# Performance work log

Measured on AMD Instinct MI355X. Metric: run time of the kernel, lower is better.

The kernel has to match this reference:

```python
import jax, jax.numpy as jnp
import numpy as np

B, C, HZ, SX = 512, 112, 8, 16
P = HZ * HZ   # num_kernel = 64 template pixels
OC = 256
EPS = 1e-5

def _conv(x, w, pad, groups=1):
    return jax.lax.conv_general_dilated(
        x, w, (1, 1), [(pad, pad), (pad, pad)],
        feature_group_count=groups,
        dimension_numbers=('NCHW', 'OIHW', 'NCHW'))

def _bn(x, g, b, m, v):
    # eval-mode BatchNorm2d with running stats
    scale = (g / jnp.sqrt(v + EPS))[None, :, None, None]
    return (x - m[None, :, None, None]) * scale + b[None, :, None, None]

def setup_inputs() -> dict:
    key = jax.random.key(0)
    ks = jax.random.split(key, 16)
    n = lambda i, shape, s=0.05: jax.random.normal(ks[i], shape, dtype=jnp.float32) * s
    return dict(
        search=jax.random.normal(ks[0], (B, C, SX, SX), dtype=jnp.float32),
        kernel=jax.random.normal(ks[1], (B, C, HZ, HZ), dtype=jnp.float32),
        ca_w1=n(2, (P, P)), ca_b1=jnp.zeros((P,), jnp.float32),
        ca_w2=n(3, (P, P)), ca_b2=jnp.zeros((P,), jnp.float32),
        cls_dw=n(4, (P, 1, 3, 3)), cls_pw=n(5, (OC, P)),
        cls_bn_g=jnp.ones((OC,), jnp.float32), cls_bn_b=jnp.zeros((OC,), jnp.float32),
        cls_bn_m=n(6, (OC,)), cls_bn_v=jax.random.uniform(ks[7], (OC,), jnp.float32, 0.5, 1.5),
        cls_pred_w=n(8, (1, OC, 3, 3)), cls_pred_b=jnp.zeros((1,), jnp.float32),
        box_dw=n(9, (P, 1, 3, 3)), box_pw=n(10, (OC, P)),
        box_bn_g=jnp.ones((OC,), jnp.float32), box_bn_b=jnp.zeros((OC,), jnp.float32),
        box_bn_m=n(11, (OC,)), box_bn_v=jax.random.uniform(ks[12], (OC,), jnp.float32, 0.5, 1.5),
        box_pred_w=n(13, (4, OC, 3, 3)), box_pred_b=jnp.zeros((4,), jnp.float32),
        adjust=0.1 * jnp.ones((1,), jnp.float32),
        bias_p=jnp.ones((1, 4, 1, 1), jnp.float32),
    )

def reference(search, kernel, ca_w1, ca_b1, ca_w2, ca_b2,
              cls_dw, cls_pw, cls_bn_g, cls_bn_b, cls_bn_m, cls_bn_v,
              cls_pred_w, cls_pred_b,
              box_dw, box_pw, box_bn_g, box_bn_b, box_bn_m, box_bn_v,
              box_pred_w, box_pred_b, adjust, bias_p):
    b, c, h, w = search.shape
    # pixel-wise correlation (batched form of the per-sample F.conv2d loop):
    # corr[b,p,i,j] = sum_c kernel[b,c].flatten()[p] * search[b,c,i,j]
    z = kernel.reshape(b, c, -1)                       # [B, C, P]
    corr = jnp.einsum('bcp,bcij->bpij', z, search)      # [B, P, H, W]
    # channel attention (CAModule, reduction=1)
    s = corr.mean(axis=(2, 3))                          # [B, P]
    a = jax.nn.sigmoid(jax.nn.relu(s @ ca_w1.T + ca_b1) @ ca_w2.T + ca_b2)
    corr = corr * a[:, :, None, None]
    # cls tower: depthwise 3x3 -> pointwise -> BN -> ReLU
    cfeat = jnp.einsum('oc,bchw->bohw', cls_pw, _conv(corr, cls_dw, 1, groups=P))
    cfeat = jax.nn.relu(_bn(cfeat, cls_bn_g, cls_bn_b, cls_bn_m, cls_bn_v))
    cls = 0.1 * (_conv(cfeat, cls_pred_w, 1) + cls_pred_b[None, :, None, None])
    # bbox tower
    rfeat = jnp.einsum('oc,bchw->bohw', box_pw, _conv(corr, box_dw, 1, groups=P))
    rfeat = jax.nn.relu(_bn(rfeat, box_bn_g, box_bn_b, box_bn_m, box_bn_v))
    pred = _conv(rfeat, box_pred_w, 1) + box_pred_b[None, :, None, None]
    x = jnp.exp(adjust[0] * pred + bias_p)
    return (x, cls)
```

## Files before the change

### kernel.cpp

```cpp
#include <hip/hip_runtime.h>
#include <hip/hip_bf16.h>


typedef __attribute__((ext_vector_type(8))) short  bf16x8;
typedef __attribute__((ext_vector_type(4))) float  f32x4;

union U8 { bf16x8 v; uint4 q; unsigned short u[8]; };

__device__ __forceinline__ float bf2f(unsigned short h){
  union { unsigned int u; float f; } c; c.u = ((unsigned int)h) << 16; return c.f;
}
__device__ __forceinline__ unsigned short f2bf(float f){
  union { float f; unsigned int u; } c; c.f = f;
  unsigned int r = (c.u + 0x7FFFu + ((c.u >> 16) & 1u)) >> 16;
  return (unsigned short)r;
}
__device__ __forceinline__ unsigned int f2bf2(float lo, float hi){
  return (unsigned int)f2bf(lo) | ((unsigned int)f2bf(hi) << 16);
}

__device__ __forceinline__ int swz(int row, int pix){
  return row*256 + (((pix>>3) ^ (row&31))<<3) + (pix&7);
}
__device__ __forceinline__ int zt_off(int p, int c){
  return (p<<8) + ((((c>>3) ^ (p&15)) & 15)<<4) + ((c&7)<<1);
}
__device__ __forceinline__ int sT_off(int pix, int c){
  return (pix<<7) + ((((c>>3) ^ (pix&7) ^ ((pix>>3)&7)) & 7)<<4) + ((c&7)<<1);
}
__device__ __forceinline__ int dT_off(int pix, int p){
  return (pix<<7) + (((((p>>3) ^ pix) & 7)) << 4) + ((p & 7) << 1);
}
__device__ __forceinline__ int fT_off(int pix, int ocl){
  return (pix<<6) + ((((ocl>>3) ^ pix ^ (pix>>2)) & 3) << 4) + ((ocl & 7) << 1);
}
__device__ __forceinline__ int pA_off(int ocl, int p){
  return (ocl<<7) + (((((p>>3) ^ ocl) & 7)) << 4) + ((p & 7) << 1);
}

__device__ __forceinline__ void stage_pw(int tid, int oc0,
                                         const float* __restrict__ pw,
                                         unsigned char* __restrict__ dst){
  const int ocl = tid >> 4, p0 = (tid & 15) << 2;
  const float4 f0 = *(const float4*)&pw[(oc0 + ocl)*64 + p0];
  uint2 w; w.x = f2bf2(f0.x, f0.y); w.y = f2bf2(f0.z, f0.w);
  *(uint2*)(dst + pA_off(ocl, p0)) = w;
}

template<int NOUT>
__device__ __forceinline__ void stage_wA(int tid, int oc0,
                                         const float* __restrict__ pdw,
                                         unsigned char* __restrict__ dst){
  #pragma unroll
  for (int i=0;i<(NOUT*288+511)/512;++i){
    const int idx = i*512 + tid;
    if (idx < NOUT*288){
      const int o   = idx / 288;
      const int rem = idx - o*288;
      const int tau = rem >> 5, ocl = rem & 31;
      *(unsigned short*)(dst + (idx<<1)) =
          f2bf(pdw[(o*256 + oc0 + ocl)*9 + tau]);
    }
  }
}

template<int NOUT>
__device__ __forceinline__ void run_tower(
    int tid, float ap,
    const float* __restrict__ dw,  const float* __restrict__ pw,
    const float* __restrict__ bng, const float* __restrict__ bnb,
    const float* __restrict__ bnm, const float* __restrict__ bnv,
    const float* __restrict__ pdw, const float* __restrict__ pdb,
    float* __restrict__ outp, float adj, const float* __restrict__ biasp,
    unsigned char* smem)
{
  const int lane = tid & 63, wave = tid >> 6;
  const int l15 = lane & 15, lg = lane >> 4;
  unsigned short* sA16 = (unsigned short*)smem;

  {
    const int p = lane;
    unsigned char* dT = smem + 32768;
    float wd[9];
    #pragma unroll
    for (int k=0;k<9;++k) wd[k] = dw[p*9+k] * ap;
    #pragma unroll
    for (int io=0;io<2;++io){
      const int ir = wave*2 + io;
      float ot[16];
      #pragma unroll
      for (int j=0;j<16;++j) ot[j] = 0.f;
      #pragma unroll
      for (int dr=0;dr<3;++dr){
        const int r = ir-1+dr;
        if (r >= 0 && r < 16){
          unsigned short tr[16];
          *(uint4*)&tr[0] = *(uint4*)&sA16[swz(p, r*16)];
          *(uint4*)&tr[8] = *(uint4*)&sA16[swz(p, r*16 + 8)];
          float rr[16];
          #pragma unroll
          for (int j=0;j<16;++j) rr[j] = bf2f(tr[j]);
          const float w0 = wd[dr*3+0], w1 = wd[dr*3+1], w2 = wd[dr*3+2];
          #pragma unroll
          for (int j=0;j<16;++j){
            float s = w1*rr[j];
            if (j > 0)  s = fmaf(w0, rr[j-1], s);
            if (j < 15) s = fmaf(w2, rr[j+1], s);
            ot[j] += s;
          }
        }
      }
      #pragma unroll
      for (int j=0;j<16;++j)
        *(unsigned short*)(dT + dT_off(ir*16+j, p)) = f2bf(ot[j]);
    }
  }
  __syncthreads();

  U8 bfr[2][2];
  #pragma unroll
  for (int nt=0;nt<2;++nt)
    #pragma unroll
    for (int ks=0;ks<2;++ks)
      bfr[nt][ks].q = *(const uint4*)(smem + 32768 +
          dT_off(wave*32 + nt*16 + l15, ks*32 + lg*8));
  __syncthreads();

  float* scl = (float*)(smem + 61952);
  float* bia = (float*)(smem + 62976);
  if (tid < 256){
    const float s = bng[tid] * rsqrtf(bnv[tid] + 1e-5f);
    scl[tid] = s;
    bia[tid] = bnb[tid] - bnm[tid]*s;
  }
  stage_pw(tid, 0, pw, smem + 49152);
  stage_wA<NOUT>(tid, 0, pdw, smem + 57344);

  f32x4 accp[2];
  #pragma unroll
  for (int nt=0;nt<2;++nt) accp[nt] = f32x4{0.f,0.f,0.f,0.f};

  for (int ch=0; ch<8; ++ch){
    const int buf = ch & 1, oc0 = ch*32;
    __syncthreads();

    unsigned char* pAb = smem + 49152 + buf*4096;
    U8 af[2][2];
    #pragma unroll
    for (int mt=0;mt<2;++mt)
      #pragma unroll
      for (int ks=0;ks<2;++ks)
        af[mt][ks].q = *(const uint4*)(pAb + pA_off(mt*16 + l15, ks*32 + lg*8));
    f32x4 accw[2][2];
    #pragma unroll
    for (int mt=0;mt<2;++mt)
      #pragma unroll
      for (int nt=0;nt<2;++nt) accw[mt][nt] = f32x4{0.f,0.f,0.f,0.f};
    #pragma unroll
    for (int nt=0;nt<2;++nt){
      #pragma unroll
      for (int mt=0;mt<2;++mt){
        accw[mt][nt] = __builtin_amdgcn_mfma_f32_16x16x32_bf16(
            af[mt][0].v, bfr[nt][0].v, accw[mt][nt], 0, 0, 0);
        accw[mt][nt] = __builtin_amdgcn_mfma_f32_16x16x32_bf16(
            af[mt][1].v, bfr[nt][1].v, accw[mt][nt], 0, 0, 0);
      }
    }
    #pragma unroll
    for (int mt=0;mt<2;++mt){
      #pragma unroll
      for (int r=0;r<4;++r){
        const int ocl = mt*16 + lg*4 + r;
        const float sc = scl[oc0+ocl], bi = bia[oc0+ocl];
        #pragma unroll
        for (int nt=0;nt<2;++nt){
          const int pix = wave*32 + nt*16 + l15;
          const float v = fmaxf(fmaf(accw[mt][nt][r], sc, bi), 0.f);
          *(unsigned short*)(smem + 32768 + fT_off(pix, ocl)) = f2bf(v);
        }
      }
    }
    __syncthreads();

    unsigned char* wAb = smem + 57344 + buf*2304;
    #pragma unroll
    for (int dr=0;dr<3;++dr){
      #pragma unroll
      for (int dc=0;dc<3;++dc){
        const int tau = dr*3 + dc;
        U8 a;
        const int mr = (NOUT == 4) ? (l15 & 3) : 0;
        a.q = *(const uint4*)(wAb + ((mr*288 + tau*32 + lg*8) << 1));
        if (l15 >= NOUT) a.q = make_uint4(0u,0u,0u,0u);
        #pragma unroll
        for (int nt=0;nt<2;++nt){
          const int rp = wave*2 + nt + dr - 1;
          if (rp >= 0 && rp <= 15){
            const int cp = l15 + dc - 1;
            const int cc = cp < 0 ? 0 : (cp > 15 ? 15 : cp);
            U8 bf;
            bf.q = *(const uint4*)(smem + 32768 + fT_off(rp*16 + cc, lg*8));
            if (cp != cc) bf.q = make_uint4(0u,0u,0u,0u);
            accp[nt] = __builtin_amdgcn_mfma_f32_16x16x32_bf16(
                a.v, bf.v, accp[nt], 0, 0, 0);
          }
        }
      }
    }
    if (ch < 7){
      stage_pw(tid, oc0 + 32, pw, smem + 49152 + (buf^1)*4096);
      stage_wA<NOUT>(tid, oc0 + 32, pdw, smem + 57344 + (buf^1)*2304);
    }
  }

  if (lane < 16){
    #pragma unroll
    for (int nt=0;nt<2;++nt){
      const int rt = wave*2 + nt;
      if constexpr (NOUT == 1){
        outp[rt*16 + lane] = 0.1f*(accp[nt][0] + pdb[0]);
      } else {
        #pragma unroll
        for (int o=0;o<4;++o)
          outp[o*256 + rt*16 + lane] =
              expf(fmaf(adj, accp[nt][o] + pdb[o], biasp[o]));
      }
    }
  }
  __syncthreads();
}

__global__ __launch_bounds__(512, 4) void fused_head(
  const float* __restrict__ search, const float* __restrict__ kern,
  const float* __restrict__ ca_w1, const float* __restrict__ ca_b1,
  const float* __restrict__ ca_w2, const float* __restrict__ ca_b2,
  const float* __restrict__ cls_dw, const float* __restrict__ cls_pw,
  const float* __restrict__ cls_bn_g, const float* __restrict__ cls_bn_b,
  const float* __restrict__ cls_bn_m, const float* __restrict__ cls_bn_v,
  const float* __restrict__ cls_pred_w, const float* __restrict__ cls_pred_b,
  const float* __restrict__ box_dw, const float* __restrict__ box_pw,
  const float* __restrict__ box_bn_g, const float* __restrict__ box_bn_b,
  const float* __restrict__ box_bn_m, const float* __restrict__ box_bn_v,
  const float* __restrict__ box_pred_w, const float* __restrict__ box_pred_b,
  const float* __restrict__ adjust, const float* __restrict__ bias_p,
  float* __restrict__ out)
{
  __shared__ __align__(16) unsigned char smem[65536];
  const int b   = blockIdx.x;
  const int tid = threadIdx.x;
  const int lane = tid & 63, wave = tid >> 6;
  const int l15 = lane & 15, lg = lane >> 4;

  unsigned char* zb = smem;
  {
    const float* kb = kern + (size_t)b*7168;
    #pragma unroll
    for (int i=0;i<14;++i){
      const int idx = i*512 + tid;
      const int c = idx>>6, p = idx&63;
      *(unsigned short*)(zb + zt_off(p,c)) = f2bf(kb[idx]);
    }
    #pragma unroll
    for (int i=0;i<2;++i){
      const int idx = i*512 + tid;
      const int p = idx>>4, c = 112 + (idx&15);
      *(unsigned short*)(zb + zt_off(p,c)) = 0;
    }
  }

  unsigned char* stb = smem + 16384;
  const float* sea = search + (size_t)b*28672;
  f32x4 acc[4][2];
  #pragma unroll
  for (int mt=0;mt<4;++mt)
    #pragma unroll
    for (int nt=0;nt<2;++nt) acc[mt][nt] = f32x4{0.f,0.f,0.f,0.f};

  for (int kc=0;kc<2;++kc){
    __syncthreads();
    #pragma unroll
    for (int i=0;i<8;++i){
      const int f4i = i*512 + tid;
      const int cc = f4i>>6, pix0 = (f4i&63)<<2;
      const int c  = kc*64 + cc;
      float4 v;
      if (c < 112) v = *(const float4*)(sea + c*256 + pix0);
      else         v = make_float4(0.f,0.f,0.f,0.f);
      const float vv[4] = {v.x, v.y, v.z, v.w};
      #pragma unroll
      for (int j=0;j<4;++j)
        *(unsigned short*)(stb + sT_off(pix0+j, cc)) = f2bf(vv[j]);
    }
    __syncthreads();
    #pragma unroll
    for (int kt=0;kt<2;++kt){
      U8 bh[2];
      #pragma unroll
      for (int nt=0;nt<2;++nt){
        const int pix = wave*32 + nt*16 + l15;
        bh[nt].q = *(const uint4*)(stb + sT_off(pix, kt*32 + lg*8));
      }
      #pragma unroll
      for (int mt=0;mt<4;++mt){
        U8 ah;
        ah.q = *(const uint4*)(zb + zt_off(mt*16 + l15, kc*64 + kt*32 + lg*8));
        #pragma unroll
        for (int nt=0;nt<2;++nt)
          acc[mt][nt] = __builtin_amdgcn_mfma_f32_16x16x32_bf16(
              ah.v, bh[nt].v, acc[mt][nt], 0, 0, 0);
      }
    }
  }
  __syncthreads();

  unsigned short* sA16 = (unsigned short*)smem;
  #pragma unroll
  for (int mt=0;mt<4;++mt){
    #pragma unroll
    for (int nt=0;nt<2;++nt){
      const int pix = wave*32 + nt*16 + l15;
      #pragma unroll
      for (int r=0;r<4;++r)
        sA16[swz(mt*16 + lg*4 + r, pix)] = f2bf(acc[mt][nt][r]);
    }
  }

  float* ws    = (float*)(smem + 49152);
  float* smean = (float*)(smem + 51200);
  float* h1    = (float*)(smem + 51456);
  float* attvG = (float*)(smem + 51712);
  #pragma unroll
  for (int mt=0;mt<4;++mt){
    #pragma unroll
    for (int r=0;r<4;++r){
      float s = acc[mt][0][r] + acc[mt][1][r];
      s += __shfl_xor(s, 1, 64);
      s += __shfl_xor(s, 2, 64);
      s += __shfl_xor(s, 4, 64);
      s += __shfl_xor(s, 8, 64);
      if (l15 == 0) ws[wave*64 + mt*16 + lg*4 + r] = s;
    }
  }
  __syncthreads();
  if (tid < 64){
    float m = 0.f;
    #pragma unroll
    for (int w=0;w<8;++w) m += ws[w*64 + tid];
    smean[tid] = m * (1.f/256.f);
  }
  __syncthreads();
  if (tid < 64){
    float s = ca_b1[tid];
    const float* wr = ca_w1 + tid*64;
    #pragma unroll 8
    for (int k=0;k<64;++k) s += smean[k]*wr[k];
    h1[tid] = fmaxf(s, 0.f);
  }
  __syncthreads();
  if (tid < 64){
    float s = ca_b2[tid];
    const float* wr = ca_w2 + tid*64;
    #pragma unroll 8
    for (int k=0;k<64;++k) s += h1[k]*wr[k];
    attvG[tid] = 1.f/(1.f + expf(-s));
  }
  __syncthreads();
  const float ap = attvG[lane];

  const float adj = adjust[0];

  run_tower<1>(tid, ap, cls_dw, cls_pw, cls_bn_g, cls_bn_b, cls_bn_m,
               cls_bn_v, cls_pred_w, cls_pred_b,
               out + 524288 + (size_t)b*256, adj, bias_p, smem);
  run_tower<4>(tid, ap, box_dw, box_pw, box_bn_g, box_bn_b, box_bn_m,
               box_bn_v, box_pred_w, box_pred_b,
               out + (size_t)b*1024, adj, bias_p, smem);
}

extern "C" void kernel_launch(void* const* d_in, const int* in_sizes, int n_in,
                              void* d_out, int out_size, void* d_ws, size_t ws_size,
                              hipStream_t stream) {
  (void)in_sizes; (void)n_in; (void)d_ws; (void)ws_size; (void)out_size;
  const float* search     = (const float*)d_in[0];
  const float* kern       = (const float*)d_in[1];
  const float* ca_w1      = (const float*)d_in[2];
  const float* ca_b1      = (const float*)d_in[3];
  const float* ca_w2      = (const float*)d_in[4];
  const float* ca_b2      = (const float*)d_in[5];
  const float* cls_dw     = (const float*)d_in[6];
  const float* cls_pw     = (const float*)d_in[7];
  const float* cls_bn_g   = (const float*)d_in[8];
  const float* cls_bn_b   = (const float*)d_in[9];
  const float* cls_bn_m   = (const float*)d_in[10];
  const float* cls_bn_v   = (const float*)d_in[11];
  const float* cls_pred_w = (const float*)d_in[12];
  const float* cls_pred_b = (const float*)d_in[13];
  const float* box_dw     = (const float*)d_in[14];
  const float* box_pw     = (const float*)d_in[15];
  const float* box_bn_g   = (const float*)d_in[16];
  const float* box_bn_b   = (const float*)d_in[17];
  const float* box_bn_m   = (const float*)d_in[18];
  const float* box_bn_v   = (const float*)d_in[19];
  const float* box_pred_w = (const float*)d_in[20];
  const float* box_pred_b = (const float*)d_in[21];
  const float* adjust     = (const float*)d_in[22];
  const float* bias_p     = (const float*)d_in[23];

  hipLaunchKernelGGL(fused_head, dim3(512), dim3(512), 0, stream,
    search, kern, ca_w1, ca_b1, ca_w2, ca_b2,
    cls_dw, cls_pw, cls_bn_g, cls_bn_b, cls_bn_m, cls_bn_v,
    cls_pred_w, cls_pred_b,
    box_dw, box_pw, box_bn_g, box_bn_b, box_bn_m, box_bn_v,
    box_pred_w, box_pred_b, adjust, bias_p,
    (float*)d_out);
}
```

Before: 71.70 us.

## Run cls and box towers concurrently on separate halves of the block

Both depthwise convolutions still use all 512 threads, one after the other. The pointwise, BN and pred-conv stages of the two towers now run at the same time, with threads 0-255 handling cls and 256-511 handling box. Each half uses its own shared-memory regions for features, weights and BN parameters, and each wave covers 64 pixels instead of 32. The aim is to cut the number of serial chunk loops and barriers by overlapping the two towers. In exchange, the block is load-imbalanced because the box half does about four times the pred work, and register pressure per thread rises.

```diff
diff --git a/kernel.cpp b/kernel.cpp
--- a/kernel.cpp
+++ b/kernel.cpp
@@ -38,196 +38,68 @@
   return (ocl<<7) + (((((p>>3) ^ ocl) & 7)) << 4) + ((p & 7) << 1);
 }
 
-__device__ __forceinline__ void stage_pw(int tid, int oc0,
-                                         const float* __restrict__ pw,
-                                         unsigned char* __restrict__ dst){
-  const int ocl = tid >> 4, p0 = (tid & 15) << 2;
+__device__ __forceinline__ void depthwise(
+    int lane, int wave, float ap, const float* __restrict__ dw,
+    const unsigned short* __restrict__ sA16, unsigned char* __restrict__ dst)
+{
+  const int p = lane;
+  float wd[9];
+  #pragma unroll
+  for (int k=0;k<9;++k) wd[k] = dw[p*9+k] * ap;
+  #pragma unroll
+  for (int io=0;io<2;++io){
+    const int ir = wave*2 + io;
+    float ot[16];
+    #pragma unroll
+    for (int j=0;j<16;++j) ot[j] = 0.f;
+    #pragma unroll
+    for (int dr=0;dr<3;++dr){
+      const int r = ir-1+dr;
+      if (r >= 0 && r < 16){
+        unsigned short tr[16];
+        *(uint4*)&tr[0] = *(uint4*)&sA16[swz(p, r*16)];
+        *(uint4*)&tr[8] = *(uint4*)&sA16[swz(p, r*16 + 8)];
+        float rr[16];
+        #pragma unroll
+        for (int j=0;j<16;++j) rr[j] = bf2f(tr[j]);
+        const float w0 = wd[dr*3+0], w1 = wd[dr*3+1], w2 = wd[dr*3+2];
+        #pragma unroll
+        for (int j=0;j<16;++j){
+          float s = w1*rr[j];
+          if (j > 0)  s = fmaf(w0, rr[j-1], s);
+          if (j < 15) s = fmaf(w2, rr[j+1], s);
+          ot[j] += s;
+        }
+      }
+    }
+    #pragma unroll
+    for (int j=0;j<16;++j)
+      *(unsigned short*)(dst + dT_off(ir*16+j, p)) = f2bf(ot[j]);
+  }
+}
+
+__device__ __forceinline__ void stage_pw256(int t, int oc0,
+                                            const float* __restrict__ pw,
+                                            unsigned char* __restrict__ dst){
+  const int ocl = t >> 3, p0 = (t & 7) << 3;
   const float4 f0 = *(const float4*)&pw[(oc0 + ocl)*64 + p0];
-  uint2 w; w.x = f2bf2(f0.x, f0.y); w.y = f2bf2(f0.z, f0.w);
-  *(uint2*)(dst + pA_off(ocl, p0)) = w;
-}
-
-template<int NOUT>
-__device__ __forceinline__ void stage_wA(int tid, int oc0,
-                                         const float* __restrict__ pdw,
-                                         unsigned char* __restrict__ dst){
-  #pragma unroll
-  for (int i=0;i<(NOUT*288+511)/512;++i){
-    const int idx = i*512 + tid;
-    if (idx < NOUT*288){
-      const int o   = idx / 288;
-      const int rem = idx - o*288;
-      const int tau = rem >> 5, ocl = rem & 31;
-      *(unsigned short*)(dst + (idx<<1)) =
-          f2bf(pdw[(o*256 + oc0 + ocl)*9 + tau]);
-    }
-  }
-}
-
-template<int NOUT>
-__device__ __forceinline__ void run_tower(
-    int tid, float ap,
-    const float* __restrict__ dw,  const float* __restrict__ pw,
-    const float* __restrict__ bng, const float* __restrict__ bnb,
-    const float* __restrict__ bnm, const float* __restrict__ bnv,
-    const float* __restrict__ pdw, const float* __restrict__ pdb,
-    float* __restrict__ outp, float adj, const float* __restrict__ biasp,
-    unsigned char* smem)
-{
-  const int lane = tid & 63, wave = tid >> 6;
-  const int l15 = lane & 15, lg = lane >> 4;
-  unsigned short* sA16 = (unsigned short*)smem;
-
-  {
-    const int p = lane;
-    unsigned char* dT = smem + 32768;
-    float wd[9];
-    #pragma unroll
-    for (int k=0;k<9;++k) wd[k] = dw[p*9+k] * ap;
-    #pragma unroll
-    for (int io=0;io<2;++io){
-      const int ir = wave*2 + io;
-      float ot[16];
-      #pragma unroll
-      for (int j=0;j<16;++j) ot[j] = 0.f;
-      #pragma unroll
-      for (int dr=0;dr<3;++dr){
-        const int r = ir-1+dr;
-        if (r >= 0 && r < 16){
-          unsigned short tr[16];
-          *(uint4*)&tr[0] = *(uint4*)&sA16[swz(p, r*16)];
-          *(uint4*)&tr[8] = *(uint4*)&sA16[swz(p, r*16 + 8)];
-          float rr[16];
-          #pragma unroll
-          for (int j=0;j<16;++j) rr[j] = bf2f(tr[j]);
-          const float w0 = wd[dr*3+0], w1 = wd[dr*3+1], w2 = wd[dr*3+2];
-          #pragma unroll
-          for (int j=0;j<16;++j){
-            float s = w1*rr[j];
-            if (j > 0)  s = fmaf(w0, rr[j-1], s);
-            if (j < 15) s = fmaf(w2, rr[j+1], s);
-            ot[j] += s;
-          }
-        }
-      }
-      #pragma unroll
-      for (int j=0;j<16;++j)
-        *(unsigned short*)(dT + dT_off(ir*16+j, p)) = f2bf(ot[j]);
-    }
-  }
-  __syncthreads();
-
-  U8 bfr[2][2];
-  #pragma unroll
-  for (int nt=0;nt<2;++nt)
-    #pragma unroll
-    for (int ks=0;ks<2;++ks)
-      bfr[nt][ks].q = *(const uint4*)(smem + 32768 +
-          dT_off(wave*32 + nt*16 + l15, ks*32 + lg*8));
-  __syncthreads();
-
-  float* scl = (float*)(smem + 61952);
-  float* bia = (float*)(smem + 62976);
-  if (tid < 256){
-    const float s = bng[tid] * rsqrtf(bnv[tid] + 1e-5f);
-    scl[tid] = s;
-    bia[tid] = bnb[tid] - bnm[tid]*s;
-  }
-  stage_pw(tid, 0, pw, smem + 49152);
-  stage_wA<NOUT>(tid, 0, pdw, smem + 57344);
-
-  f32x4 accp[2];
-  #pragma unroll
-  for (int nt=0;nt<2;++nt) accp[nt] = f32x4{0.f,0.f,0.f,0.f};
-
-  for (int ch=0; ch<8; ++ch){
-    const int buf = ch & 1, oc0 = ch*32;
-    __syncthreads();
-
-    unsigned char* pAb = smem + 49152 + buf*4096;
-    U8 af[2][2];
-    #pragma unroll
-    for (int mt=0;mt<2;++mt)
-      #pragma unroll
-      for (int ks=0;ks<2;++ks)
-        af[mt][ks].q = *(const uint4*)(pAb + pA_off(mt*16 + l15, ks*32 + lg*8));
-    f32x4 accw[2][2];
-    #pragma unroll
-    for (int mt=0;mt<2;++mt)
-      #pragma unroll
-      for (int nt=0;nt<2;++nt) accw[mt][nt] = f32x4{0.f,0.f,0.f,0.f};
-    #pragma unroll
-    for (int nt=0;nt<2;++nt){
-      #pragma unroll
-      for (int mt=0;mt<2;++mt){
-        accw[mt][nt] = __builtin_amdgcn_mfma_f32_16x16x32_bf16(
-            af[mt][0].v, bfr[nt][0].v, accw[mt][nt], 0, 0, 0);
-        accw[mt][nt] = __builtin_amdgcn_mfma_f32_16x16x32_bf16(
-            af[mt][1].v, bfr[nt][1].v, accw[mt][nt], 0, 0, 0);
-      }
-    }
-    #pragma unroll
-    for (int mt=0;mt<2;++mt){
-      #pragma unroll
-      for (int r=0;r<4;++r){
-        const int ocl = mt*16 + lg*4 + r;
-        const float sc = scl[oc0+ocl], bi = bia[oc0+ocl];
-        #pragma unroll
-        for (int nt=0;nt<2;++nt){
-          const int pix = wave*32 + nt*16 + l15;
-          const float v = fmaxf(fmaf(accw[mt][nt][r], sc, bi), 0.f);
-          *(unsigned short*)(smem + 32768 + fT_off(pix, ocl)) = f2bf(v);
-        }
-      }
-    }
-    __syncthreads();
-
-    unsigned char* wAb = smem + 57344 + buf*2304;
-    #pragma unroll
-    for (int dr=0;dr<3;++dr){
-      #pragma unroll
-      for (int dc=0;dc<3;++dc){
-        const int tau = dr*3 + dc;
-        U8 a;
-        const int mr = (NOUT == 4) ? (l15 & 3) : 0;
-        a.q = *(const uint4*)(wAb + ((mr*288 + tau*32 + lg*8) << 1));
-        if (l15 >= NOUT) a.q = make_uint4(0u,0u,0u,0u);
-        #pragma unroll
-        for (int nt=0;nt<2;++nt){
-          const int rp = wave*2 + nt + dr - 1;
-          if (rp >= 0 && rp <= 15){
-            const int cp = l15 + dc - 1;
-            const int cc = cp < 0 ? 0 : (cp > 15 ? 15 : cp);
-            U8 bf;
-            bf.q = *(const uint4*)(smem + 32768 + fT_off(rp*16 + cc, lg*8));
-            if (cp != cc) bf.q = make_uint4(0u,0u,0u,0u);
-            accp[nt] = __builtin_amdgcn_mfma_f32_16x16x32_bf16(
-                a.v, bf.v, accp[nt], 0, 0, 0);
-          }
-        }
-      }
-    }
-    if (ch < 7){
-      stage_pw(tid, oc0 + 32, pw, smem + 49152 + (buf^1)*4096);
-      stage_wA<NOUT>(tid, oc0 + 32, pdw, smem + 57344 + (buf^1)*2304);
-    }
-  }
-
-  if (lane < 16){
-    #pragma unroll
-    for (int nt=0;nt<2;++nt){
-      const int rt = wave*2 + nt;
-      if constexpr (NOUT == 1){
-        outp[rt*16 + lane] = 0.1f*(accp[nt][0] + pdb[0]);
-      } else {
-        #pragma unroll
-        for (int o=0;o<4;++o)
-          outp[o*256 + rt*16 + lane] =
-              expf(fmaf(adj, accp[nt][o] + pdb[o], biasp[o]));
-      }
-    }
-  }
-  __syncthreads();
+  const float4 f1 = *(const float4*)&pw[(oc0 + ocl)*64 + p0 + 4];
+  U8 w;
+  w.u[0]=f2bf(f0.x); w.u[1]=f2bf(f0.y); w.u[2]=f2bf(f0.z); w.u[3]=f2bf(f0.w);
+  w.u[4]=f2bf(f1.x); w.u[5]=f2bf(f1.y); w.u[6]=f2bf(f1.z); w.u[7]=f2bf(f1.w);
+  *(uint4*)(dst + pA_off(ocl, p0)) = w.q;
+}
+
+__device__ __forceinline__ void stage_wA256(int t, int oc0, int nout,
+                                            const float* __restrict__ pdw,
+                                            unsigned char* __restrict__ dst){
+  for (int idx = t; idx < nout*288; idx += 256){
+    const int o   = idx / 288;
+    const int rem = idx - o*288;
+    const int tau = rem >> 5, ocl = rem & 31;
+    *(unsigned short*)(dst + (idx<<1)) =
+        f2bf(pdw[(o*256 + oc0 + ocl)*9 + tau]);
+  }
 }
 
 __global__ __launch_bounds__(512, 4) void fused_head(
@@ -366,15 +238,157 @@
   }
   __syncthreads();
   const float ap = attvG[lane];
+  __syncthreads();
 
   const float adj = adjust[0];
 
-  run_tower<1>(tid, ap, cls_dw, cls_pw, cls_bn_g, cls_bn_b, cls_bn_m,
-               cls_bn_v, cls_pred_w, cls_pred_b,
-               out + 524288 + (size_t)b*256, adj, bias_p, smem);
-  run_tower<4>(tid, ap, box_dw, box_pw, box_bn_g, box_bn_b, box_bn_m,
-               box_bn_v, box_pred_w, box_pred_b,
-               out + (size_t)b*1024, adj, bias_p, smem);
+  const int half = tid >> 8;
+  const int ttid = tid & 255;
+  const int wt   = wave & 3;
+  const int nout = half ? 4 : 1;
+
+  const float* pwp  = half ? box_pw     : cls_pw;
+  const float* bngp = half ? box_bn_g   : cls_bn_g;
+  const float* bnbp = half ? box_bn_b   : cls_bn_b;
+  const float* bnmp = half ? box_bn_m   : cls_bn_m;
+  const float* bnvp = half ? box_bn_v   : cls_bn_v;
+  const float* pdwp = half ? box_pred_w : cls_pred_w;
+  const float* pdbp = half ? box_pred_b : cls_pred_b;
+  float* outp = half ? (out + (size_t)b*1024)
+                     : (out + 524288 + (size_t)b*256);
+
+  unsigned char* dT = smem + 32768;
+
+  depthwise(lane, wave, ap, cls_dw, sA16, dT);
+  __syncthreads();
+  U8 bfr[4][2];
+  if (half == 0){
+    #pragma unroll
+    for (int nt=0;nt<4;++nt)
+      #pragma unroll
+      for (int ks=0;ks<2;++ks)
+        bfr[nt][ks].q = *(const uint4*)(dT +
+            dT_off(wt*64 + nt*16 + l15, ks*32 + lg*8));
+  }
+  __syncthreads();
+  depthwise(lane, wave, ap, box_dw, sA16, dT);
+  __syncthreads();
+  if (half == 1){
+    #pragma unroll
+    for (int nt=0;nt<4;++nt)
+      #pragma unroll
+      for (int ks=0;ks<2;++ks)
+        bfr[nt][ks].q = *(const uint4*)(dT +
+            dT_off(wt*64 + nt*16 + l15, ks*32 + lg*8));
+  }
+  __syncthreads();
+
+  unsigned char* featb = smem + half*16384;
+  unsigned char* pwb0  = smem + 32768 + half*8192;
+  unsigned char* wab0  = smem + (half ? 50304 : 49152);
+  const int wstride = nout*576;
+  float* scl = (float*)(smem + 55296 + half*2048);
+  float* bia = scl + 256;
+
+  {
+    const float s = bngp[ttid] * rsqrtf(bnvp[ttid] + 1e-5f);
+    scl[ttid] = s;
+    bia[ttid] = bnbp[ttid] - bnmp[ttid]*s;
+  }
+  stage_pw256(ttid, 0, pwp, pwb0);
+  stage_wA256(ttid, 0, nout, pdwp, wab0);
+
+  f32x4 accp[4];
+  #pragma unroll
+  for (int nt=0;nt<4;++nt) accp[nt] = f32x4{0.f,0.f,0.f,0.f};
+
+  for (int ch=0; ch<8; ++ch){
+    const int buf = ch & 1, oc0 = ch*32;
+    __syncthreads();
+
+    unsigned char* pAb = pwb0 + buf*4096;
+    U8 af[2][2];
+    #pragma unroll
+    for (int mt=0;mt<2;++mt)
+      #pragma unroll
+      for (int ks=0;ks<2;++ks)
+        af[mt][ks].q = *(const uint4*)(pAb + pA_off(mt*16 + l15, ks*32 + lg*8));
+    f32x4 accw[2][4];
+    #pragma unroll
+    for (int mt=0;mt<2;++mt)
+      #pragma unroll
+      for (int nt=0;nt<4;++nt) accw[mt][nt] = f32x4{0.f,0.f,0.f,0.f};
+    #pragma unroll
+    for (int nt=0;nt<4;++nt){
+      #pragma unroll
+      for (int mt=0;mt<2;++mt){
+        accw[mt][nt] = __builtin_amdgcn_mfma_f32_16x16x32_bf16(
+            af[mt][0].v, bfr[nt][0].v, accw[mt][nt], 0, 0, 0);
+        accw[mt][nt] = __builtin_amdgcn_mfma_f32_16x16x32_bf16(
+            af[mt][1].v, bfr[nt][1].v, accw[mt][nt], 0, 0, 0);
+      }
+    }
+    #pragma unroll
+    for (int mt=0;mt<2;++mt){
+      #pragma unroll
+      for (int r=0;r<4;++r){
+        const int ocl = mt*16 + lg*4 + r;
+        const float sc = scl[oc0+ocl], bi = bia[oc0+ocl];
+        #pragma unroll
+        for (int nt=0;nt<4;++nt){
+          const int pix = wt*64 + nt*16 + l15;
+          const float v = fmaxf(fmaf(accw[mt][nt][r], sc, bi), 0.f);
+          *(unsigned short*)(featb + fT_off(pix, ocl)) = f2bf(v);
+        }
+      }
+    }
+    __syncthreads();
+
+    unsigned char* wAb = wab0 + buf*wstride;
+    #pragma unroll
+    for (int dr=0;dr<3;++dr){
+      #pragma unroll
+      for (int dc=0;dc<3;++dc){
+        const int tau = dr*3 + dc;
+        U8 a;
+        const int mr = (nout == 4) ? (l15 & 3) : 0;
+        a.q = *(const uint4*)(wAb + ((mr*288 + tau*32 + lg*8) << 1));
+        if (l15 >= nout) a.q = make_uint4(0u,0u,0u,0u);
+        #pragma unroll
+        for (int nt=0;nt<4;++nt){
+          const int rp = wt*4 + nt + dr - 1;
+          if (rp >= 0 && rp <= 15){
+            const int cp = l15 + dc - 1;
+            const int cc = cp < 0 ? 0 : (cp > 15 ? 15 : cp);
+            U8 bf;
+            bf.q = *(const uint4*)(featb + fT_off(rp*16 + cc, lg*8));
+            if (cp != cc) bf.q = make_uint4(0u,0u,0u,0u);
+            accp[nt] = __builtin_amdgcn_mfma_f32_16x16x32_bf16(
+                a.v, bf.v, accp[nt], 0, 0, 0);
+          }
+        }
+      }
+    }
+    if (ch < 7){
+      stage_pw256(ttid, oc0 + 32, pwp, pwb0 + (buf^1)*4096);
+      stage_wA256(ttid, oc0 + 32, nout, pdwp, wab0 + (buf^1)*wstride);
+    }
+  }
+
+  if (lane < 16){
+    #pragma unroll
+    for (int nt=0;nt<4;++nt){
+      const int rt = wt*4 + nt;
+      if (nout == 1){
+        outp[rt*16 + lane] = 0.1f*(accp[nt][0] + pdbp[0]);
+      } else {
+        #pragma unroll
+        for (int o=0;o<4;++o)
+          outp[o*256 + rt*16 + lane] =
+              expf(fmaf(adj, accp[nt][o] + pdbp[o], bias_p[o]));
+      }
+    }
+  }
 }
 
 extern "C" void kernel_launch(void* const* d_in, const int* in_sizes, int n_in,
```

After: 77.18 us. 1.08x slower.

## Software-pipeline pointwise and 3x3 pred stages with double-buffered feature tiles

Applied to the files above, without the earlier changes.

The pointwise+BN+ReLU chunk for the next 32 output channels is now computed into a second feature buffer while the 3x3 prediction MFMAs consume the current one. This removes one barrier per chunk. The correlation tile is kept in registers as packed bf16 and rewritten to shared memory at the start of each tower, which frees shared space for the second feature buffer. In exchange it raises register pressure and adds an LDS rewrite per tower.

```diff
diff --git a/kernel.cpp b/kernel.cpp
--- a/kernel.cpp
+++ b/kernel.cpp
@@ -66,7 +66,7 @@
 
 template<int NOUT>
 __device__ __forceinline__ void run_tower(
-    int tid, float ap,
+    int tid, float ap, const unsigned int pk[16],
     const float* __restrict__ dw,  const float* __restrict__ pw,
     const float* __restrict__ bng, const float* __restrict__ bnb,
     const float* __restrict__ bnm, const float* __restrict__ bnv,
@@ -77,6 +77,22 @@
   const int lane = tid & 63, wave = tid >> 6;
   const int l15 = lane & 15, lg = lane >> 4;
   unsigned short* sA16 = (unsigned short*)smem;
+
+  #pragma unroll
+  for (int mt=0;mt<4;++mt){
+    #pragma unroll
+    for (int nt=0;nt<2;++nt){
+      const int pix = wave*32 + nt*16 + l15;
+      #pragma unroll
+      for (int rp=0;rp<2;++rp){
+        const unsigned int v = pk[(mt*2+nt)*2+rp];
+        const int p = mt*16 + lg*4 + rp*2;
+        sA16[swz(p,   pix)] = (unsigned short)(v & 0xffffu);
+        sA16[swz(p+1, pix)] = (unsigned short)(v >> 16);
+      }
+    }
+  }
+  __syncthreads();
 
   {
     const int p = lane;
@@ -133,41 +149,30 @@
     scl[tid] = s;
     bia[tid] = bnb[tid] - bnm[tid]*s;
   }
-  stage_pw(tid, 0, pw, smem + 49152);
+  stage_pw(tid, 0,  pw, smem + 49152);
+  stage_pw(tid, 32, pw, smem + 53248);
   stage_wA<NOUT>(tid, 0, pdw, smem + 57344);
-
-  f32x4 accp[2];
-  #pragma unroll
-  for (int nt=0;nt<2;++nt) accp[nt] = f32x4{0.f,0.f,0.f,0.f};
-
-  for (int ch=0; ch<8; ++ch){
-    const int buf = ch & 1, oc0 = ch*32;
-    __syncthreads();
-
-    unsigned char* pAb = smem + 49152 + buf*4096;
-    U8 af[2][2];
-    #pragma unroll
-    for (int mt=0;mt<2;++mt)
-      #pragma unroll
-      for (int ks=0;ks<2;++ks)
-        af[mt][ks].q = *(const uint4*)(pAb + pA_off(mt*16 + l15, ks*32 + lg*8));
-    f32x4 accw[2][2];
-    #pragma unroll
-    for (int mt=0;mt<2;++mt)
-      #pragma unroll
-      for (int nt=0;nt<2;++nt) accw[mt][nt] = f32x4{0.f,0.f,0.f,0.f};
-    #pragma unroll
-    for (int nt=0;nt<2;++nt){
-      #pragma unroll
-      for (int mt=0;mt<2;++mt){
-        accw[mt][nt] = __builtin_amdgcn_mfma_f32_16x16x32_bf16(
-            af[mt][0].v, bfr[nt][0].v, accw[mt][nt], 0, 0, 0);
-        accw[mt][nt] = __builtin_amdgcn_mfma_f32_16x16x32_bf16(
-            af[mt][1].v, bfr[nt][1].v, accw[mt][nt], 0, 0, 0);
-      }
-    }
+  __syncthreads();
+
+  auto pw_chunk = [&](int c){
+    unsigned char* pAb   = smem + 49152 + (c&1)*4096;
+    unsigned char* featb = smem + (c&1)*16384;
+    const int oc0 = c*32;
     #pragma unroll
     for (int mt=0;mt<2;++mt){
+      U8 af0, af1;
+      af0.q = *(const uint4*)(pAb + pA_off(mt*16 + l15, lg*8));
+      af1.q = *(const uint4*)(pAb + pA_off(mt*16 + l15, 32 + lg*8));
+      f32x4 accw[2];
+      accw[0] = f32x4{0.f,0.f,0.f,0.f};
+      accw[1] = f32x4{0.f,0.f,0.f,0.f};
+      #pragma unroll
+      for (int nt=0;nt<2;++nt){
+        accw[nt] = __builtin_amdgcn_mfma_f32_16x16x32_bf16(
+            af0.v, bfr[nt][0].v, accw[nt], 0, 0, 0);
+        accw[nt] = __builtin_amdgcn_mfma_f32_16x16x32_bf16(
+            af1.v, bfr[nt][1].v, accw[nt], 0, 0, 0);
+      }
       #pragma unroll
       for (int r=0;r<4;++r){
         const int ocl = mt*16 + lg*4 + r;
@@ -175,14 +180,28 @@
         #pragma unroll
         for (int nt=0;nt<2;++nt){
           const int pix = wave*32 + nt*16 + l15;
-          const float v = fmaxf(fmaf(accw[mt][nt][r], sc, bi), 0.f);
-          *(unsigned short*)(smem + 32768 + fT_off(pix, ocl)) = f2bf(v);
+          const float v = fmaxf(fmaf(accw[nt][r], sc, bi), 0.f);
+          *(unsigned short*)(featb + fT_off(pix, ocl)) = f2bf(v);
         }
       }
     }
-    __syncthreads();
-
-    unsigned char* wAb = smem + 57344 + buf*2304;
+  };
+
+  pw_chunk(0);
+  __syncthreads();
+
+  f32x4 accp[2];
+  accp[0] = f32x4{0.f,0.f,0.f,0.f};
+  accp[1] = f32x4{0.f,0.f,0.f,0.f};
+
+  for (int i=0; i<8; ++i){
+    if (i < 6) stage_pw(tid, (i+2)*32, pw, smem + 49152 + (i&1)*4096);
+    if (i < 7) stage_wA<NOUT>(tid, (i+1)*32, pdw,
+                              smem + 57344 + ((i+1)&1)*2304);
+    if (i < 7) pw_chunk(i+1);
+
+    unsigned char* featb = smem + (i&1)*16384;
+    unsigned char* wAb   = smem + 57344 + (i&1)*2304;
     #pragma unroll
     for (int dr=0;dr<3;++dr){
       #pragma unroll
@@ -199,7 +218,7 @@
             const int cp = l15 + dc - 1;
             const int cc = cp < 0 ? 0 : (cp > 15 ? 15 : cp);
             U8 bf;
-            bf.q = *(const uint4*)(smem + 32768 + fT_off(rp*16 + cc, lg*8));
+            bf.q = *(const uint4*)(featb + fT_off(rp*16 + cc, lg*8));
             if (cp != cc) bf.q = make_uint4(0u,0u,0u,0u);
             accp[nt] = __builtin_amdgcn_mfma_f32_16x16x32_bf16(
                 a.v, bf.v, accp[nt], 0, 0, 0);
@@ -207,10 +226,7 @@
         }
       }
     }
-    if (ch < 7){
-      stage_pw(tid, oc0 + 32, pw, smem + 49152 + (buf^1)*4096);
-      stage_wA<NOUT>(tid, oc0 + 32, pdw, smem + 57344 + (buf^1)*2304);
-    }
+    __syncthreads();
   }
 
   if (lane < 16){
@@ -227,7 +243,6 @@
       }
     }
   }
-  __syncthreads();
 }
 
 __global__ __launch_bounds__(512, 4) void fused_head(
@@ -313,18 +328,6 @@
   }
   __syncthreads();
 
-  unsigned short* sA16 = (unsigned short*)smem;
-  #pragma unroll
-  for (int mt=0;mt<4;++mt){
-    #pragma unroll
-    for (int nt=0;nt<2;++nt){
-      const int pix = wave*32 + nt*16 + l15;
-      #pragma unroll
-      for (int r=0;r<4;++r)
-        sA16[swz(mt*16 + lg*4 + r, pix)] = f2bf(acc[mt][nt][r]);
-    }
-  }
-
   float* ws    = (float*)(smem + 49152);
   float* smean = (float*)(smem + 51200);
   float* h1    = (float*)(smem + 51456);
@@ -341,6 +344,14 @@
       if (l15 == 0) ws[wave*64 + mt*16 + lg*4 + r] = s;
     }
   }
+  unsigned int pk[16];
+  #pragma unroll
+  for (int mt=0;mt<4;++mt)
+    #pragma unroll
+    for (int nt=0;nt<2;++nt)
+      #pragma unroll
+      for (int rp=0;rp<2;++rp)
+        pk[(mt*2+nt)*2+rp] = f2bf2(acc[mt][nt][rp*2], acc[mt][nt][rp*2+1]);
   __syncthreads();
   if (tid < 64){
     float m = 0.f;
@@ -366,13 +377,15 @@
   }
   __syncthreads();
   const float ap = attvG[lane];
+  __syncthreads();
 
   const float adj = adjust[0];
 
-  run_tower<1>(tid, ap, cls_dw, cls_pw, cls_bn_g, cls_bn_b, cls_bn_m,
+  run_tower<1>(tid, ap, pk, cls_dw, cls_pw, cls_bn_g, cls_bn_b, cls_bn_m,
                cls_bn_v, cls_pred_w, cls_pred_b,
                out + 524288 + (size_t)b*256, adj, bias_p, smem);
-  run_tower<4>(tid, ap, box_dw, box_pw, box_bn_g, box_bn_b, box_bn_m,
+  __syncthreads();
+  run_tower<4>(tid, ap, pk, box_dw, box_pw, box_bn_g, box_bn_b, box_bn_m,
                box_bn_v, box_pred_w, box_pred_b,
                out + (size_t)b*1024, adj, bias_p, smem);
 }
```

Result: slower. 94.13 us (+31.3%).
